# Kernel tuning notes

Measured on AMD Instinct MI355X. Metric: run time of the kernel, lower is better.

The kernel has to match this reference:

```python
import jax, jax.numpy as jnp
import numpy as np

EPS_BN = 1e-5


def conv2d(x, w, b, stride=1, pad=0):
    y = jax.lax.conv_general_dilated(
        x, w, (stride, stride), [(pad, pad), (pad, pad)],
        dimension_numbers=('NCHW', 'OIHW', 'NCHW'))
    return y + b[None, :, None, None]


def resize_ac(x, oh, ow):
    # bilinear resize, align_corners=True (matches F.interpolate(..., align_corners=True))
    N, C, H, W = x.shape
    ys = jnp.linspace(0.0, H - 1.0, oh)
    xs = jnp.linspace(0.0, W - 1.0, ow)
    y0 = jnp.floor(ys).astype(jnp.int32)
    x0 = jnp.floor(xs).astype(jnp.int32)
    y1 = jnp.minimum(y0 + 1, H - 1)
    x1 = jnp.minimum(x0 + 1, W - 1)
    wy = (ys - y0)[None, None, :, None]
    wx = (xs - x0)[None, None, None, :]
    top = jnp.take(x, y0, axis=2)
    bot = jnp.take(x, y1, axis=2)
    rows = top * (1.0 - wy) + bot * wy
    left = jnp.take(rows, x0, axis=3)
    right = jnp.take(rows, x1, axis=3)
    return left * (1.0 - wx) + right * wx


def grid_sample_3d(vol, grid):
    # vol: (N,C,D,H,W); grid: (N,Do,Ho,Wo,3) with channels (x->W, y->H, z->D)
    # trilinear, padding_mode='zeros', align_corners=False (torch defaults)
    N, C, D, H, W = vol.shape
    out_shape = grid.shape[1:4]
    gx = grid[..., 0].reshape(N, -1)
    gy = grid[..., 1].reshape(N, -1)
    gz = grid[..., 2].reshape(N, -1)
    ix = ((gx + 1.0) * W - 1.0) * 0.5
    iy = ((gy + 1.0) * H - 1.0) * 0.5
    iz = ((gz + 1.0) * D - 1.0) * 0.5
    x0 = jnp.floor(ix); y0 = jnp.floor(iy); z0 = jnp.floor(iz)
    fx = ix - x0; fy = iy - y0; fz = iz - z0
    volf = vol.reshape(N, C, D * H * W)

    def corner(xi, yi, zi, wgt):
        valid = ((xi >= 0) & (xi < W) & (yi >= 0) & (yi < H) & (zi >= 0) & (zi < D))
        xc = jnp.clip(xi, 0, W - 1).astype(jnp.int32)
        yc = jnp.clip(yi, 0, H - 1).astype(jnp.int32)
        zc = jnp.clip(zi, 0, D - 1).astype(jnp.int32)
        lin = (zc * H + yc) * W + xc  # (N,P)
        g = jnp.take_along_axis(volf, lin[:, None, :], axis=2)  # (N,C,P)
        return g * (wgt * valid.astype(vol.dtype))[:, None, :]

    out = 0.0
    for zi, wz in ((z0, 1.0 - fz), (z0 + 1.0, fz)):
        for yi, wy in ((y0, 1.0 - fy), (y0 + 1.0, fy)):
            for xi, wx in ((x0, 1.0 - fx), (x0 + 1.0, fx)):
                out = out + corner(xi, yi, zi, wz * wy * wx)
    return out.reshape(N, C, *out_shape)


def setup_inputs() -> dict:
    key = jax.random.key(0)
    ks = jax.random.split(key, 9)
    N, H, W = 1, 2048, 2048
    f = lambda k, shp, s: jax.random.normal(k, shp, jnp.float32) * s
    return dict(
        low=jax.random.uniform(ks[0], (N, 3, H, W), jnp.float32),
        med=jax.random.uniform(ks[1], (N, 3, H, W), jnp.float32),
        high=jax.random.uniform(ks[2], (N, 3, H, W), jnp.float32),
        w1=f(ks[3], (16, 9, 3, 3), 0.1), b1=jnp.zeros((16,), jnp.float32),
        w2=f(ks[4], (32, 16, 3, 3), 0.1), b2=jnp.zeros((32,), jnp.float32),
        w3=f(ks[5], (64, 32, 3, 3), 0.1), b3=jnp.zeros((64,), jnp.float32),
        w4=f(ks[6], (192, 64, 1, 1), 0.1), b4=jnp.zeros((192,), jnp.float32),
        gw1=f(ks[7], (16, 3, 1, 1), 0.3), gb1=jnp.zeros((16,), jnp.float32),
        g_gamma=jnp.ones((16,), jnp.float32), g_beta=jnp.zeros((16,), jnp.float32),
        g_mean=jnp.zeros((16,), jnp.float32), g_var=jnp.ones((16,), jnp.float32),
        gw2=f(ks[8], (1, 16, 1, 1), 0.3), gb2=jnp.zeros((1,), jnp.float32),
    )


def _forward(low, med, high, w1, b1, w2, b2, w3, b3, w4, b4,
             gw1, gb1, g_gamma, g_beta, g_mean, g_var, gw2, gb2):
    img = 0.33 * low + 0.33 * med + 0.33 * high  # (N,3,H,W)

    # ---- Coeffs: downsample 9-ch input to 128x128, run coeff net -> (N,12,16,16,16)
    x = resize_ac(jnp.concatenate([low, med, high], axis=1), 128, 128)
    x = jax.nn.relu(conv2d(x, w1, b1, stride=2, pad=1))   # 64x64
    x = jax.nn.relu(conv2d(x, w2, b2, stride=2, pad=1))   # 32x32
    x = jax.nn.relu(conv2d(x, w3, b3, stride=2, pad=1))   # 16x16
    coeff = conv2d(x, w4, b4, stride=1, pad=0)            # (N,192,16,16)
    grid_vol = coeff.reshape(-1, 12, 16, 16, 16)          # (N,12,D,H,W)

    # ---- GuideNN at full res: 1x1 conv -> BN(eval) -> ReLU -> 1x1 conv -> sigmoid
    g = conv2d(img, gw1, gb1)
    g = g_gamma[None, :, None, None] * (g - g_mean[None, :, None, None]) \
        * jax.lax.rsqrt(g_var[None, :, None, None] + EPS_BN) + g_beta[None, :, None, None]
    g = jax.nn.relu(g)
    guide = jax.nn.sigmoid(conv2d(g, gw2, gb2))           # (N,1,H,W)
    guide = resize_ac(guide, 64, 64)[:, 0]                # (N,64,64)

    # ---- Slice: trilinear lookup into bilateral grid, guided by (guide, hg, wg)
    N = guide.shape[0]
    lin = (jnp.arange(64, dtype=jnp.float32) / 63.0) * 2.0 - 1.0
    hg = jnp.broadcast_to(lin[:, None], (64, 64))
    wg = jnp.broadcast_to(lin[None, :], (64, 64))
    grid = jnp.stack([guide,
                      jnp.broadcast_to(hg, guide.shape),
                      jnp.broadcast_to(wg, guide.shape)], axis=-1)[:, None]  # (N,1,64,64,3)
    sc = grid_sample_3d(grid_vol, grid)[:, :, 0]          # (N,12,64,64)

    # ---- Apply: upsample coeffs to full res, per-pixel 3x4 affine (HDRNet apply)
    Hi, Wi = img.shape[2], img.shape[3]
    cf = resize_ac(sc, Hi, Wi).reshape(N, 3, 4, Hi, Wi)
    out = jnp.einsum('ncjhw,njhw->nchw', cf[:, :, :3], img) + cf[:, :, 3]
    return out


def reference(low, med, high, w1, b1, w2, b2, w3, b3, w4, b4,
              gw1, gb1, g_gamma, g_beta, g_mean, g_var, gw2, gb2):
    return _forward(low, med, high, w1, b1, w2, b2, w3, b3, w4, b4,
                    gw1, gb1, g_gamma, g_beta, g_mean, g_var, gw2, gb2)
```

## Files before the change

### kernel.cpp

```cpp
#include <hip/hip_runtime.h>
#include <math.h>

#define HH 2048
#define WW 2048
#define HWFULL (HH*WW)

typedef float v4f __attribute__((ext_vector_type(4)));
union F4 { float4 v; v4f c; float f[4]; };

__global__ __launch_bounds__(256) void k_conv1(const float* __restrict__ low,
                                               const float* __restrict__ med,
                                               const float* __restrict__ high,
                                               const float* __restrict__ w,
                                               const float* __restrict__ b,
                                               float* __restrict__ out) {
    __shared__ float sd[9 * 3 * 34];
    const int oy = blockIdx.x >> 2;
    const int q  = blockIdx.x & 3;
    const int tid = threadIdx.x;
    for (int idx = tid; idx < 9 * 3 * 33; idx += 256) {
        int ch = idx / 99;
        int rem = idx - 99 * ch;
        int r = rem / 33;
        int j = rem - 33 * r;
        int ix128 = 32 * q - 1 + j;
        int iy128 = 2 * oy - 1 + r;
        float val = 0.0f;
        if (ix128 >= 0 && ix128 < 128 && iy128 >= 0 && iy128 < 128) {
            const float* base = (ch < 3) ? low : (ch < 6 ? med : high);
            const float* p = base + (ch % 3) * HWFULL;
            float ysf = iy128 * (2047.0f / 127.0f);
            int y0 = (int)ysf; if (y0 > 2047) y0 = 2047;
            int y1 = y0 + 1;   if (y1 > 2047) y1 = 2047;
            float wy = ysf - (float)y0;
            float xsf = ix128 * (2047.0f / 127.0f);
            int x0 = (int)xsf; if (x0 > 2047) x0 = 2047;
            int x1 = x0 + 1;   if (x1 > 2047) x1 = 2047;
            float wx = xsf - (float)x0;
            float t = p[y0 * WW + x0] * (1.0f - wx) + p[y0 * WW + x1] * wx;
            float bo = p[y1 * WW + x0] * (1.0f - wx) + p[y1 * WW + x1] * wx;
            val = t * (1.0f - wy) + bo * wy;
        }
        sd[(ch * 3 + r) * 34 + j] = val;
    }
    __syncthreads();
    int co = tid >> 4, xl = tid & 15;
    float acc = b[co];
    for (int ci = 0; ci < 9; ++ci) {
        #pragma unroll
        for (int ky = 0; ky < 3; ++ky) {
            const float* wr = w + ((co * 9 + ci) * 3 + ky) * 3;
            const float* row = &sd[(ci * 3 + ky) * 34 + 2 * xl];
            acc += wr[0] * row[0] + wr[1] * row[1] + wr[2] * row[2];
        }
    }
    out[co * 4096 + oy * 64 + 16 * q + xl] = fmaxf(acc, 0.0f);
}

__global__ __launch_bounds__(256) void k_conv2(const float* __restrict__ in,
                                               const float* __restrict__ w,
                                               const float* __restrict__ b,
                                               const float* __restrict__ low,
                                               const float* __restrict__ med,
                                               const float* __restrict__ high,
                                               const float* __restrict__ gw1, const float* __restrict__ gb1,
                                               const float* __restrict__ gamma, const float* __restrict__ beta,
                                               const float* __restrict__ mean, const float* __restrict__ var,
                                               const float* __restrict__ gw2, const float* __restrict__ gb2,
                                               float* __restrict__ out,
                                               float* __restrict__ guideb) {
    __shared__ float sd[16 * 3 * 18];
    const int oy = blockIdx.x >> 2;
    const int q  = blockIdx.x & 3;
    const int tid = threadIdx.x;
    for (int idx = tid; idx < 16 * 3 * 17; idx += 256) {
        int ch = idx / 51;
        int rem = idx - 51 * ch;
        int r = rem / 17;
        int j = rem - 17 * r;
        int x = 16 * q - 1 + j;
        int iy = 2 * oy - 1 + r;
        sd[(ch * 3 + r) * 18 + j] =
            (x >= 0 && x < 64 && iy >= 0 && iy < 64) ? in[ch * 4096 + iy * 64 + x] : 0.0f;
    }
    __syncthreads();
    int co = tid >> 3, xl = tid & 7;
    float acc = b[co];
    for (int ci = 0; ci < 16; ++ci) {
        #pragma unroll
        for (int ky = 0; ky < 3; ++ky) {
            const float* wr = w + ((co * 16 + ci) * 3 + ky) * 3;
            const float* row = &sd[(ci * 3 + ky) * 18 + 2 * xl];
            acc += wr[0] * row[0] + wr[1] * row[1] + wr[2] * row[2];
        }
    }
    out[co * 1024 + oy * 32 + 8 * q + xl] = fmaxf(acc, 0.0f);

    if (tid < 32) {
        int g = blockIdx.x * 32 + tid;
        int h = g >> 6, wv = g & 63;
        float ysf = h * (2047.0f / 63.0f);
        int y0 = (int)ysf; if (y0 > 2047) y0 = 2047;
        int y1 = y0 + 1;   if (y1 > 2047) y1 = 2047;
        float wy = ysf - (float)y0;
        float xsf = wv * (2047.0f / 63.0f);
        int x0 = (int)xsf; if (x0 > 2047) x0 = 2047;
        int x1 = x0 + 1;   if (x1 > 2047) x1 = 2047;
        float wx = xsf - (float)x0;
        int yy[2] = { y0, y1 };
        int xx[2] = { x0, x1 };
        float gp[2][2];
        #pragma unroll
        for (int a = 0; a < 2; ++a) {
            #pragma unroll
            for (int bb = 0; bb < 2; ++bb) {
                int pix = yy[a] * WW + xx[bb];
                float i0 = 0.33f * (low[pix]            + med[pix]            + high[pix]);
                float i1 = 0.33f * (low[HWFULL + pix]   + med[HWFULL + pix]   + high[HWFULL + pix]);
                float i2 = 0.33f * (low[2*HWFULL + pix] + med[2*HWFULL + pix] + high[2*HWFULL + pix]);
                float acc2 = gb2[0];
                for (int k = 0; k < 16; ++k) {
                    float t = gb1[k] + gw1[k*3] * i0 + gw1[k*3+1] * i1 + gw1[k*3+2] * i2;
                    t = gamma[k] * (t - mean[k]) * (1.0f / sqrtf(var[k] + 1e-5f)) + beta[k];
                    t = fmaxf(t, 0.0f);
                    acc2 += gw2[k] * t;
                }
                gp[a][bb] = 1.0f / (1.0f + expf(-acc2));
            }
        }
        guideb[g] = (1.0f - wy) * ((1.0f - wx) * gp[0][0] + wx * gp[0][1])
                  +         wy  * ((1.0f - wx) * gp[1][0] + wx * gp[1][1]);
    }
}

__global__ __launch_bounds__(256) void k_conv34(const float* __restrict__ in,
                                                const float* __restrict__ w3,
                                                const float* __restrict__ b3,
                                                const float* __restrict__ w4,
                                                const float* __restrict__ b4,
                                                float* __restrict__ gridvol) {
    __shared__ float sd[32 * 3 * 10];
    __shared__ float sc3[64 * 4];
    const int oy = blockIdx.x >> 2;
    const int q  = blockIdx.x & 3;
    const int tid = threadIdx.x;
    for (int idx = tid; idx < 32 * 3 * 9; idx += 256) {
        int ch = idx / 27;
        int rem = idx - 27 * ch;
        int r = rem / 9;
        int j = rem - 9 * r;
        int x = 8 * q - 1 + j;
        int iy = 2 * oy - 1 + r;
        sd[(ch * 3 + r) * 10 + j] =
            (x >= 0 && x < 32 && iy >= 0 && iy < 32) ? in[ch * 1024 + iy * 32 + x] : 0.0f;
    }
    __syncthreads();
    {
        int co = tid >> 2, xl = tid & 3;
        float acc = b3[co];
        for (int ci = 0; ci < 32; ++ci) {
            #pragma unroll
            for (int ky = 0; ky < 3; ++ky) {
                const float* wr = w3 + ((co * 32 + ci) * 3 + ky) * 3;
                const float* row = &sd[(ci * 3 + ky) * 10 + 2 * xl];
                acc += wr[0] * row[0] + wr[1] * row[1] + wr[2] * row[2];
            }
        }
        sc3[co * 4 + xl] = fmaxf(acc, 0.0f);
    }
    __syncthreads();
    {
        int px = tid & 3;
        int ob = tid >> 2;
        #pragma unroll
        for (int k = 0; k < 3; ++k) {
            int o = ob + 64 * k;
            float sum = b4[o];
            const float* wp = w4 + o * 64;
            for (int i = 0; i < 64; ++i)
                sum += wp[i] * sc3[i * 4 + px];
            gridvol[o * 256 + oy * 16 + 4 * q + px] = sum;
        }
    }
}

__global__ __launch_bounds__(256) void k_slice_ab(
        const float* __restrict__ gridvol, const float* __restrict__ guideb,
        float* __restrict__ ab_full) {
    __shared__ float s[3 * 64 * 12];
    const int b = blockIdx.x;
    const int tid = threadIdx.x;
    float byf = (8 * b) * (63.0f / 2047.0f);
    int v0 = (int)byf; if (v0 > 63) v0 = 63;

    if (tid < 192) {
        int rr = tid >> 6, x = tid & 63;
        int srow = v0 + rr; if (srow > 63) srow = 63;
        float guide = guideb[srow * 64 + x];
        float hg = srow * (2.0f / 63.0f) - 1.0f;
        float wg = x * (2.0f / 63.0f) - 1.0f;
        float ix = ((guide + 1.0f) * 16.0f - 1.0f) * 0.5f;
        float iy = ((hg    + 1.0f) * 16.0f - 1.0f) * 0.5f;
        float iz = ((wg    + 1.0f) * 16.0f - 1.0f) * 0.5f;
        float xf = floorf(ix), yf = floorf(iy), zf = floorf(iz);
        float fx = ix - xf, fyy = iy - yf, fz = iz - zf;
        int xi = (int)xf, yi = (int)yf, zi = (int)zf;
        float scv[12];
        #pragma unroll
        for (int c = 0; c < 12; ++c) scv[c] = 0.0f;
        #pragma unroll
        for (int dz = 0; dz < 2; ++dz) {
            int z = zi + dz; float wz = dz ? fz : 1.0f - fz;
            if (z < 0 || z > 15) continue;
            #pragma unroll
            for (int dy = 0; dy < 2; ++dy) {
                int yv = yi + dy; float wyv = dy ? fyy : 1.0f - fyy;
                if (yv < 0 || yv > 15) continue;
                #pragma unroll
                for (int dx = 0; dx < 2; ++dx) {
                    int xv = xi + dx; float wxv = dx ? fx : 1.0f - fx;
                    if (xv < 0 || xv > 15) continue;
                    float wgt = wz * wyv * wxv;
                    int base = yv * 16 + xv;
                    #pragma unroll
                    for (int c = 0; c < 12; ++c)
                        scv[c] += wgt * gridvol[(c * 16 + z) * 256 + base];
                }
            }
        }
        #pragma unroll
        for (int c = 0; c < 12; ++c) s[(rr * 64 + x) * 12 + c] = scv[c];
    }
    __syncthreads();

    #pragma unroll
    for (int k = 0; k < 24; ++k) {
        int e = k * 256 + tid;
        int r8 = e / 768;
        int rem = e - 768 * r8;
        int x = rem / 12;
        int c = rem - 12 * x;
        int y = 8 * b + r8;
        float iyf = y * (63.0f / 2047.0f);
        int y0 = (int)iyf; if (y0 > 63) y0 = 63;
        int y1 = y0 + 1;   if (y1 > 63) y1 = 63;
        float fy = iyf - (float)y0;
        int i0 = y0 - v0, i1 = y1 - v0;
        float t = s[(i0 * 64 + x) * 12 + c];
        float bo = s[(i1 * 64 + x) * 12 + c];
        ab_full[y * 768 + rem] = t + (bo - t) * fy;
    }
}

__global__ __launch_bounds__(256) void k_apply(
        const float* __restrict__ low, const float* __restrict__ med,
        const float* __restrict__ high, const float* __restrict__ ab_full,
        float* __restrict__ out) {
    const int g = blockIdx.x * 256 + threadIdx.x;
    const int y = g >> 9;
    const int v = g & 511;
    const int HW4 = HWFULL / 4;

    const float4* Lp = (const float4*)low;
    const float4* Mp = (const float4*)med;
    const float4* Hp = (const float4*)high;

    F4 l0, l1, l2, m0, m1, m2, h0, h1, h2;
    l0.v = Lp[g]; l1.v = Lp[g + HW4]; l2.v = Lp[g + 2 * HW4];
    m0.v = Mp[g]; m1.v = Mp[g + HW4]; m2.v = Mp[g + 2 * HW4];
    h0.v = Hp[g]; h1.v = Hp[g + HW4]; h2.v = Hp[g + 2 * HW4];

    const float4* abr = (const float4*)(ab_full + y * 768);
    int x_first = v << 2;
    float ixf0 = x_first * (63.0f / 2047.0f);
    int f = (int)ixf0; if (f > 63) f = 63;
    float ixf3 = (x_first + 3) * (63.0f / 2047.0f);
    int s3 = (int)ixf3; if (s3 > 63) s3 = 63;
    int fp1 = f + 1;  if (fp1 > 63) fp1 = 63;
    int sp1 = s3 + 1; if (sp1 > 63) sp1 = 63;
    F4 A0[3], B0[3], C0[3];
    #pragma unroll
    for (int qq = 0; qq < 3; ++qq) {
        A0[qq].v = abr[f   * 3 + qq];
        B0[qq].v = abr[fp1 * 3 + qq];
        C0[qq].v = abr[sp1 * 3 + qq];
    }

    F4 o0, o1, o2;
    #pragma unroll
    for (int p = 0; p < 4; ++p) {
        int x = x_first + p;
        float ixf = x * (63.0f / 2047.0f);
        int x0 = (int)ixf; if (x0 > 63) x0 = 63;
        float fx = ixf - (float)x0;
        bool first = (x0 == f);
        float im0 = 0.33f * (l0.f[p] + m0.f[p] + h0.f[p]);
        float im1 = 0.33f * (l1.f[p] + m1.f[p] + h1.f[p]);
        float im2 = 0.33f * (l2.f[p] + m2.f[p] + h2.f[p]);
        float cf[12];
        #pragma unroll
        for (int qq = 0; qq < 3; ++qq) {
            #pragma unroll
            for (int r = 0; r < 4; ++r) {
                float a = first ? A0[qq].f[r] : B0[qq].f[r];
                float bb = first ? B0[qq].f[r] : C0[qq].f[r];
                cf[qq * 4 + r] = a + (bb - a) * fx;
            }
        }
        o0.f[p] = cf[0] * im0 + cf[1]  * im1 + cf[2]  * im2 + cf[3];
        o1.f[p] = cf[4] * im0 + cf[5]  * im1 + cf[6]  * im2 + cf[7];
        o2.f[p] = cf[8] * im0 + cf[9]  * im1 + cf[10] * im2 + cf[11];
    }
    float4* Op = (float4*)out;
    Op[g]           = o0.v;
    Op[g + HW4]     = o1.v;
    Op[g + 2 * HW4] = o2.v;
}

extern "C" void kernel_launch(void* const* d_in, const int* in_sizes, int n_in,
                              void* d_out, int out_size, void* d_ws, size_t ws_size,
                              hipStream_t stream) {
    const float* low   = (const float*)d_in[0];
    const float* med   = (const float*)d_in[1];
    const float* high  = (const float*)d_in[2];
    const float* w1    = (const float*)d_in[3];
    const float* b1    = (const float*)d_in[4];
    const float* w2    = (const float*)d_in[5];
    const float* b2    = (const float*)d_in[6];
    const float* w3    = (const float*)d_in[7];
    const float* b3    = (const float*)d_in[8];
    const float* w4    = (const float*)d_in[9];
    const float* b4    = (const float*)d_in[10];
    const float* gw1   = (const float*)d_in[11];
    const float* gb1   = (const float*)d_in[12];
    const float* gamma = (const float*)d_in[13];
    const float* beta  = (const float*)d_in[14];
    const float* mean  = (const float*)d_in[15];
    const float* var   = (const float*)d_in[16];
    const float* gw2   = (const float*)d_in[17];
    const float* gb2   = (const float*)d_in[18];
    float* out = (float*)d_out;

    float* ws      = (float*)d_ws;
    float* ab_full = ws;
    float* c1      = ab_full + 1572864;
    float* c2v     = c1 + 65536;
    float* gridvol = c2v + 32768;
    float* guideb  = gridvol + 49152;

    hipLaunchKernelGGL(k_conv1,    dim3(256), dim3(256), 0, stream,
                       low, med, high, w1, b1, c1);
    hipLaunchKernelGGL(k_conv2,    dim3(128), dim3(256), 0, stream,
                       c1, w2, b2, low, med, high,
                       gw1, gb1, gamma, beta, mean, var, gw2, gb2, c2v, guideb);
    hipLaunchKernelGGL(k_conv34,   dim3(64),  dim3(256), 0, stream, c2v, w3, b3, w4, b4, gridvol);
    hipLaunchKernelGGL(k_slice_ab, dim3(256), dim3(256), 0, stream, gridvol, guideb, ab_full);
    hipLaunchKernelGGL(k_apply,    dim3(4096), dim3(256), 0, stream, low, med, high, ab_full, out);
}
```

Baseline: 81.20 us.

## Restructure apply kernel: one row per block, stage coeffs and image in LDS

The apply kernel now processes one full image row per block, staging that row's 192 coefficient float4s and the averaged 3-channel intensity in shared memory before computing outputs. Input loads and output stores use nontemporal builtins, and the grid is halved to 2048 blocks with two float4 outputs per thread. The aim is to cut redundant global reads of the coefficient row and reduce cache pollution on the streaming image traffic. In exchange it adds a block-wide barrier and extra LDS traffic.

```diff
diff --git a/kernel.cpp b/kernel.cpp
--- a/kernel.cpp
+++ b/kernel.cpp
@@ -256,65 +256,89 @@
         const float* __restrict__ low, const float* __restrict__ med,
         const float* __restrict__ high, const float* __restrict__ ab_full,
         float* __restrict__ out) {
-    const int g = blockIdx.x * 256 + threadIdx.x;
-    const int y = g >> 9;
-    const int v = g & 511;
+    __shared__ F4 img[3][512];
+    __shared__ F4 abs4[192];
+    const int y = blockIdx.x;
+    const int tid = threadIdx.x;
     const int HW4 = HWFULL / 4;
-
-    const float4* Lp = (const float4*)low;
-    const float4* Mp = (const float4*)med;
-    const float4* Hp = (const float4*)high;
-
-    F4 l0, l1, l2, m0, m1, m2, h0, h1, h2;
-    l0.v = Lp[g]; l1.v = Lp[g + HW4]; l2.v = Lp[g + 2 * HW4];
-    m0.v = Mp[g]; m1.v = Mp[g + HW4]; m2.v = Mp[g + 2 * HW4];
-    h0.v = Hp[g]; h1.v = Hp[g + HW4]; h2.v = Hp[g + 2 * HW4];
-
-    const float4* abr = (const float4*)(ab_full + y * 768);
-    int x_first = v << 2;
-    float ixf0 = x_first * (63.0f / 2047.0f);
-    int f = (int)ixf0; if (f > 63) f = 63;
-    float ixf3 = (x_first + 3) * (63.0f / 2047.0f);
-    int s3 = (int)ixf3; if (s3 > 63) s3 = 63;
-    int fp1 = f + 1;  if (fp1 > 63) fp1 = 63;
-    int sp1 = s3 + 1; if (sp1 > 63) sp1 = 63;
-    F4 A0[3], B0[3], C0[3];
+    const int base = y << 9;
+
+    const v4f* Lp = (const v4f*)low;
+    const v4f* Mp = (const v4f*)med;
+    const v4f* Hp = (const v4f*)high;
+
+    if (tid < 192)
+        abs4[tid].v = ((const float4*)(ab_full + y * 768))[tid];
+
     #pragma unroll
-    for (int qq = 0; qq < 3; ++qq) {
-        A0[qq].v = abr[f   * 3 + qq];
-        B0[qq].v = abr[fp1 * 3 + qq];
-        C0[qq].v = abr[sp1 * 3 + qq];
-    }
-
-    F4 o0, o1, o2;
+    for (int ch = 0; ch < 3; ++ch) {
+        int vi = base + ch * HW4 + tid;
+        F4 a, b, g, d, e, h;
+        a.c = __builtin_nontemporal_load(Lp + vi);
+        b.c = __builtin_nontemporal_load(Mp + vi);
+        g.c = __builtin_nontemporal_load(Hp + vi);
+        d.c = __builtin_nontemporal_load(Lp + vi + 256);
+        e.c = __builtin_nontemporal_load(Mp + vi + 256);
+        h.c = __builtin_nontemporal_load(Hp + vi + 256);
+        F4 r0, r1;
+        #pragma unroll
+        for (int p = 0; p < 4; ++p) {
+            r0.f[p] = 0.33f * (a.f[p] + b.f[p] + g.f[p]);
+            r1.f[p] = 0.33f * (d.f[p] + e.f[p] + h.f[p]);
+        }
+        img[ch][tid] = r0;
+        img[ch][tid + 256] = r1;
+        __builtin_amdgcn_sched_barrier(0);
+    }
+    __syncthreads();
+
+    v4f* Op = (v4f*)out;
     #pragma unroll
-    for (int p = 0; p < 4; ++p) {
-        int x = x_first + p;
-        float ixf = x * (63.0f / 2047.0f);
-        int x0 = (int)ixf; if (x0 > 63) x0 = 63;
-        float fx = ixf - (float)x0;
-        bool first = (x0 == f);
-        float im0 = 0.33f * (l0.f[p] + m0.f[p] + h0.f[p]);
-        float im1 = 0.33f * (l1.f[p] + m1.f[p] + h1.f[p]);
-        float im2 = 0.33f * (l2.f[p] + m2.f[p] + h2.f[p]);
-        float cf[12];
+    for (int q = 0; q < 2; ++q) {
+        int v = tid + q * 256;
+        int vi = base + v;
+        int x_first = v << 2;
+        float ixf0 = x_first * (63.0f / 2047.0f);
+        int f = (int)ixf0; if (f > 63) f = 63;
+        float ixf3 = (x_first + 3) * (63.0f / 2047.0f);
+        int s3 = (int)ixf3; if (s3 > 63) s3 = 63;
+        int fp1 = f + 1;  if (fp1 > 63) fp1 = 63;
+        int sp1 = s3 + 1; if (sp1 > 63) sp1 = 63;
+        F4 A0[3], B0[3], C0[3];
         #pragma unroll
         for (int qq = 0; qq < 3; ++qq) {
+            A0[qq] = abs4[f   * 3 + qq];
+            B0[qq] = abs4[fp1 * 3 + qq];
+            C0[qq] = abs4[sp1 * 3 + qq];
+        }
+        F4 i0 = img[0][v], i1 = img[1][v], i2 = img[2][v];
+
+        F4 o0, o1, o2;
+        #pragma unroll
+        for (int p = 0; p < 4; ++p) {
+            int x = x_first + p;
+            float ixf = x * (63.0f / 2047.0f);
+            int x0 = (int)ixf; if (x0 > 63) x0 = 63;
+            float fx = ixf - (float)x0;
+            bool first = (x0 == f);
+            float cf[12];
             #pragma unroll
-            for (int r = 0; r < 4; ++r) {
-                float a = first ? A0[qq].f[r] : B0[qq].f[r];
-                float bb = first ? B0[qq].f[r] : C0[qq].f[r];
-                cf[qq * 4 + r] = a + (bb - a) * fx;
+            for (int qq = 0; qq < 3; ++qq) {
+                #pragma unroll
+                for (int r = 0; r < 4; ++r) {
+                    float a = first ? A0[qq].f[r] : B0[qq].f[r];
+                    float bb = first ? B0[qq].f[r] : C0[qq].f[r];
+                    cf[qq * 4 + r] = a + (bb - a) * fx;
+                }
             }
-        }
-        o0.f[p] = cf[0] * im0 + cf[1]  * im1 + cf[2]  * im2 + cf[3];
-        o1.f[p] = cf[4] * im0 + cf[5]  * im1 + cf[6]  * im2 + cf[7];
-        o2.f[p] = cf[8] * im0 + cf[9]  * im1 + cf[10] * im2 + cf[11];
-    }
-    float4* Op = (float4*)out;
-    Op[g]           = o0.v;
-    Op[g + HW4]     = o1.v;
-    Op[g + 2 * HW4] = o2.v;
+            o0.f[p] = cf[0] * i0.f[p] + cf[1]  * i1.f[p] + cf[2]  * i2.f[p] + cf[3];
+            o1.f[p] = cf[4] * i0.f[p] + cf[5]  * i1.f[p] + cf[6]  * i2.f[p] + cf[7];
+            o2.f[p] = cf[8] * i0.f[p] + cf[9]  * i1.f[p] + cf[10] * i2.f[p] + cf[11];
+        }
+        __builtin_nontemporal_store(o0.c, Op + vi);
+        __builtin_nontemporal_store(o1.c, Op + vi + HW4);
+        __builtin_nontemporal_store(o2.c, Op + vi + 2 * HW4);
+    }
 }
 
 extern "C" void kernel_launch(void* const* d_in, const int* in_sizes, int n_in,
@@ -355,5 +379,5 @@
                        gw1, gb1, gamma, beta, mean, var, gw2, gb2, c2v, guideb);
     hipLaunchKernelGGL(k_conv34,   dim3(64),  dim3(256), 0, stream, c2v, w3, b3, w4, b4, gridvol);
     hipLaunchKernelGGL(k_slice_ab, dim3(256), dim3(256), 0, stream, gridvol, guideb, ab_full);
-    hipLaunchKernelGGL(k_apply,    dim3(4096), dim3(256), 0, stream, low, med, high, ab_full, out);
-}
+    hipLaunchKernelGGL(k_apply,    dim3(2048), dim3(256), 0, stream, low, med, high, ab_full, out);
+}
```

Result: slower. 87.33 us (+7.5%).

## Fuse conv1-conv4 into one halo-recomputing kernel and move guide into slice

Applied to the files above, without the earlier changes.

Merges the three conv kernels into a single 64-block kernel where each block recomputes its receptive-field halo (downsample, conv1, conv2) in shared memory before conv3 and the 1x1 conv4. The guide-network evaluation moves into k_slice_ab, so each slice block computes the guide values it needs instead of reading them from a buffer. This removes two launches and the global round trips for c1, c2 and guideb. In exchange it adds redundant halo compute, runs only 64 blocks for the conv chain, and repeats guide evaluations across neighbouring slice blocks.

```diff
diff --git a/kernel.cpp b/kernel.cpp
--- a/kernel.cpp
+++ b/kernel.cpp
@@ -8,105 +8,158 @@
 typedef float v4f __attribute__((ext_vector_type(4)));
 union F4 { float4 v; v4f c; float f[4]; };
 
-__global__ __launch_bounds__(256) void k_conv1(const float* __restrict__ low,
-                                               const float* __restrict__ med,
-                                               const float* __restrict__ high,
-                                               const float* __restrict__ w,
-                                               const float* __restrict__ b,
-                                               float* __restrict__ out) {
-    __shared__ float sd[9 * 3 * 34];
+__device__ __forceinline__ float bilin(const float* __restrict__ p, int yy, int xx,
+                                       float scale) {
+    float ysf = yy * scale;
+    int y0 = (int)ysf; if (y0 > 2047) y0 = 2047;
+    int y1 = y0 + 1;   if (y1 > 2047) y1 = 2047;
+    float wy = ysf - (float)y0;
+    float xsf = xx * scale;
+    int x0 = (int)xsf; if (x0 > 2047) x0 = 2047;
+    int x1 = x0 + 1;   if (x1 > 2047) x1 = 2047;
+    float wx = xsf - (float)x0;
+    float t = p[y0 * WW + x0] * (1.0f - wx) + p[y0 * WW + x1] * wx;
+    float b = p[y1 * WW + x0] * (1.0f - wx) + p[y1 * WW + x1] * wx;
+    return t * (1.0f - wy) + b * wy;
+}
+
+__global__ __launch_bounds__(256) void k_coeff(
+        const float* __restrict__ low, const float* __restrict__ med,
+        const float* __restrict__ high,
+        const float* __restrict__ w1, const float* __restrict__ b1,
+        const float* __restrict__ w2, const float* __restrict__ b2,
+        const float* __restrict__ w3, const float* __restrict__ b3,
+        const float* __restrict__ w4, const float* __restrict__ b4,
+        float* __restrict__ gridvol) {
+    __shared__ float ds9s[9][15][40];
+    __shared__ float c1s[16][7][20];
+    __shared__ float c2s[32][3][10];
+    __shared__ float c3s[64][4];
     const int oy = blockIdx.x >> 2;
     const int q  = blockIdx.x & 3;
     const int tid = threadIdx.x;
-    for (int idx = tid; idx < 9 * 3 * 33; idx += 256) {
-        int ch = idx / 99;
-        int rem = idx - 99 * ch;
-        int r = rem / 33;
-        int j = rem - 33 * r;
-        int ix128 = 32 * q - 1 + j;
-        int iy128 = 2 * oy - 1 + r;
+
+    for (int idx = tid; idx < 9 * 15 * 39; idx += 256) {
+        int ch = idx / 585;
+        int rem = idx - 585 * ch;
+        int r = rem / 39;
+        int j = rem - 39 * r;
+        int yy = 8 * oy - 7 + r;
+        int xx = 32 * q - 7 + j;
         float val = 0.0f;
-        if (ix128 >= 0 && ix128 < 128 && iy128 >= 0 && iy128 < 128) {
+        if (yy >= 0 && yy < 128 && xx >= 0 && xx < 128) {
             const float* base = (ch < 3) ? low : (ch < 6 ? med : high);
-            const float* p = base + (ch % 3) * HWFULL;
-            float ysf = iy128 * (2047.0f / 127.0f);
-            int y0 = (int)ysf; if (y0 > 2047) y0 = 2047;
-            int y1 = y0 + 1;   if (y1 > 2047) y1 = 2047;
-            float wy = ysf - (float)y0;
-            float xsf = ix128 * (2047.0f / 127.0f);
-            int x0 = (int)xsf; if (x0 > 2047) x0 = 2047;
-            int x1 = x0 + 1;   if (x1 > 2047) x1 = 2047;
-            float wx = xsf - (float)x0;
-            float t = p[y0 * WW + x0] * (1.0f - wx) + p[y0 * WW + x1] * wx;
-            float bo = p[y1 * WW + x0] * (1.0f - wx) + p[y1 * WW + x1] * wx;
-            val = t * (1.0f - wy) + bo * wy;
-        }
-        sd[(ch * 3 + r) * 34 + j] = val;
-    }
-    __syncthreads();
-    int co = tid >> 4, xl = tid & 15;
-    float acc = b[co];
-    for (int ci = 0; ci < 9; ++ci) {
-        #pragma unroll
-        for (int ky = 0; ky < 3; ++ky) {
-            const float* wr = w + ((co * 9 + ci) * 3 + ky) * 3;
-            const float* row = &sd[(ci * 3 + ky) * 34 + 2 * xl];
-            acc += wr[0] * row[0] + wr[1] * row[1] + wr[2] * row[2];
-        }
-    }
-    out[co * 4096 + oy * 64 + 16 * q + xl] = fmaxf(acc, 0.0f);
-}
-
-__global__ __launch_bounds__(256) void k_conv2(const float* __restrict__ in,
-                                               const float* __restrict__ w,
-                                               const float* __restrict__ b,
-                                               const float* __restrict__ low,
-                                               const float* __restrict__ med,
-                                               const float* __restrict__ high,
-                                               const float* __restrict__ gw1, const float* __restrict__ gb1,
-                                               const float* __restrict__ gamma, const float* __restrict__ beta,
-                                               const float* __restrict__ mean, const float* __restrict__ var,
-                                               const float* __restrict__ gw2, const float* __restrict__ gb2,
-                                               float* __restrict__ out,
-                                               float* __restrict__ guideb) {
-    __shared__ float sd[16 * 3 * 18];
-    const int oy = blockIdx.x >> 2;
-    const int q  = blockIdx.x & 3;
+            val = bilin(base + (ch % 3) * HWFULL, yy, xx, 2047.0f / 127.0f);
+        }
+        ds9s[ch][r][j] = val;
+    }
+    __syncthreads();
+
+    for (int v = tid; v < 16 * 7 * 19; v += 256) {
+        int co = v / 133;
+        int rem = v - 133 * co;
+        int r = rem / 19;
+        int x = rem - 19 * r;
+        int Y = 4 * oy - 3 + r;
+        int X = 16 * q - 3 + x;
+        float val = 0.0f;
+        if (Y >= 0 && Y < 64 && X >= 0 && X < 64) {
+            float acc = b1[co];
+            for (int ci = 0; ci < 9; ++ci) {
+                #pragma unroll
+                for (int ky = 0; ky < 3; ++ky) {
+                    const float* wr = w1 + ((co * 9 + ci) * 3 + ky) * 3;
+                    const float* row = &ds9s[ci][2 * r + ky][2 * x];
+                    acc += wr[0] * row[0] + wr[1] * row[1] + wr[2] * row[2];
+                }
+            }
+            val = fmaxf(acc, 0.0f);
+        }
+        c1s[co][r][x] = val;
+    }
+    __syncthreads();
+
+    for (int v = tid; v < 32 * 3 * 9; v += 256) {
+        int co = v / 27;
+        int rem = v - 27 * co;
+        int r = rem / 9;
+        int x = rem - 9 * r;
+        int Y = 2 * oy - 1 + r;
+        int X = 8 * q - 1 + x;
+        float val = 0.0f;
+        if (Y >= 0 && Y < 32 && X >= 0 && X < 32) {
+            float acc = b2[co];
+            for (int ci = 0; ci < 16; ++ci) {
+                #pragma unroll
+                for (int ky = 0; ky < 3; ++ky) {
+                    const float* wr = w2 + ((co * 16 + ci) * 3 + ky) * 3;
+                    const float* row = &c1s[ci][2 * r + ky][2 * x];
+                    acc += wr[0] * row[0] + wr[1] * row[1] + wr[2] * row[2];
+                }
+            }
+            val = fmaxf(acc, 0.0f);
+        }
+        c2s[co][r][x] = val;
+    }
+    __syncthreads();
+
+    {
+        int co = tid >> 2, xl = tid & 3;
+        float acc = b3[co];
+        for (int ci = 0; ci < 32; ++ci) {
+            #pragma unroll
+            for (int ky = 0; ky < 3; ++ky) {
+                const float* wr = w3 + ((co * 32 + ci) * 3 + ky) * 3;
+                const float* row = &c2s[ci][ky][2 * xl];
+                acc += wr[0] * row[0] + wr[1] * row[1] + wr[2] * row[2];
+            }
+        }
+        c3s[co][xl] = fmaxf(acc, 0.0f);
+    }
+    __syncthreads();
+
+    {
+        int px = tid & 3;
+        int ob = tid >> 2;
+        #pragma unroll
+        for (int k = 0; k < 3; ++k) {
+            int o = ob + 64 * k;
+            float sum = b4[o];
+            const float* wp = w4 + o * 64;
+            for (int i = 0; i < 64; ++i)
+                sum += wp[i] * c3s[i][px];
+            gridvol[o * 256 + oy * 16 + 4 * q + px] = sum;
+        }
+    }
+}
+
+__global__ __launch_bounds__(256) void k_slice_ab(
+        const float* __restrict__ gridvol,
+        const float* __restrict__ low, const float* __restrict__ med,
+        const float* __restrict__ high,
+        const float* __restrict__ gw1, const float* __restrict__ gb1,
+        const float* __restrict__ gamma, const float* __restrict__ beta,
+        const float* __restrict__ mean, const float* __restrict__ var,
+        const float* __restrict__ gw2, const float* __restrict__ gb2,
+        float* __restrict__ ab_full) {
+    __shared__ float s[3 * 64 * 12];
+    const int b = blockIdx.x;
     const int tid = threadIdx.x;
-    for (int idx = tid; idx < 16 * 3 * 17; idx += 256) {
-        int ch = idx / 51;
-        int rem = idx - 51 * ch;
-        int r = rem / 17;
-        int j = rem - 17 * r;
-        int x = 16 * q - 1 + j;
-        int iy = 2 * oy - 1 + r;
-        sd[(ch * 3 + r) * 18 + j] =
-            (x >= 0 && x < 64 && iy >= 0 && iy < 64) ? in[ch * 4096 + iy * 64 + x] : 0.0f;
-    }
-    __syncthreads();
-    int co = tid >> 3, xl = tid & 7;
-    float acc = b[co];
-    for (int ci = 0; ci < 16; ++ci) {
-        #pragma unroll
-        for (int ky = 0; ky < 3; ++ky) {
-            const float* wr = w + ((co * 16 + ci) * 3 + ky) * 3;
-            const float* row = &sd[(ci * 3 + ky) * 18 + 2 * xl];
-            acc += wr[0] * row[0] + wr[1] * row[1] + wr[2] * row[2];
-        }
-    }
-    out[co * 1024 + oy * 32 + 8 * q + xl] = fmaxf(acc, 0.0f);
-
-    if (tid < 32) {
-        int g = blockIdx.x * 32 + tid;
-        int h = g >> 6, wv = g & 63;
-        float ysf = h * (2047.0f / 63.0f);
+    float byf = (8 * b) * (63.0f / 2047.0f);
+    int v0 = (int)byf; if (v0 > 63) v0 = 63;
+
+    if (tid < 192) {
+        int rr = tid >> 6, x = tid & 63;
+        int srow = v0 + rr; if (srow > 63) srow = 63;
+
+        float ysf = srow * (2047.0f / 63.0f);
         int y0 = (int)ysf; if (y0 > 2047) y0 = 2047;
         int y1 = y0 + 1;   if (y1 > 2047) y1 = 2047;
-        float wy = ysf - (float)y0;
-        float xsf = wv * (2047.0f / 63.0f);
+        float wyg = ysf - (float)y0;
+        float xsf = x * (2047.0f / 63.0f);
         int x0 = (int)xsf; if (x0 > 2047) x0 = 2047;
         int x1 = x0 + 1;   if (x1 > 2047) x1 = 2047;
-        float wx = xsf - (float)x0;
+        float wxg = xsf - (float)x0;
         int yy[2] = { y0, y1 };
         int xx[2] = { x0, x1 };
         float gp[2][2];
@@ -128,75 +181,9 @@
                 gp[a][bb] = 1.0f / (1.0f + expf(-acc2));
             }
         }
-        guideb[g] = (1.0f - wy) * ((1.0f - wx) * gp[0][0] + wx * gp[0][1])
-                  +         wy  * ((1.0f - wx) * gp[1][0] + wx * gp[1][1]);
-    }
-}
-
-__global__ __launch_bounds__(256) void k_conv34(const float* __restrict__ in,
-                                                const float* __restrict__ w3,
-                                                const float* __restrict__ b3,
-                                                const float* __restrict__ w4,
-                                                const float* __restrict__ b4,
-                                                float* __restrict__ gridvol) {
-    __shared__ float sd[32 * 3 * 10];
-    __shared__ float sc3[64 * 4];
-    const int oy = blockIdx.x >> 2;
-    const int q  = blockIdx.x & 3;
-    const int tid = threadIdx.x;
-    for (int idx = tid; idx < 32 * 3 * 9; idx += 256) {
-        int ch = idx / 27;
-        int rem = idx - 27 * ch;
-        int r = rem / 9;
-        int j = rem - 9 * r;
-        int x = 8 * q - 1 + j;
-        int iy = 2 * oy - 1 + r;
-        sd[(ch * 3 + r) * 10 + j] =
-            (x >= 0 && x < 32 && iy >= 0 && iy < 32) ? in[ch * 1024 + iy * 32 + x] : 0.0f;
-    }
-    __syncthreads();
-    {
-        int co = tid >> 2, xl = tid & 3;
-        float acc = b3[co];
-        for (int ci = 0; ci < 32; ++ci) {
-            #pragma unroll
-            for (int ky = 0; ky < 3; ++ky) {
-                const float* wr = w3 + ((co * 32 + ci) * 3 + ky) * 3;
-                const float* row = &sd[(ci * 3 + ky) * 10 + 2 * xl];
-                acc += wr[0] * row[0] + wr[1] * row[1] + wr[2] * row[2];
-            }
-        }
-        sc3[co * 4 + xl] = fmaxf(acc, 0.0f);
-    }
-    __syncthreads();
-    {
-        int px = tid & 3;
-        int ob = tid >> 2;
-        #pragma unroll
-        for (int k = 0; k < 3; ++k) {
-            int o = ob + 64 * k;
-            float sum = b4[o];
-            const float* wp = w4 + o * 64;
-            for (int i = 0; i < 64; ++i)
-                sum += wp[i] * sc3[i * 4 + px];
-            gridvol[o * 256 + oy * 16 + 4 * q + px] = sum;
-        }
-    }
-}
-
-__global__ __launch_bounds__(256) void k_slice_ab(
-        const float* __restrict__ gridvol, const float* __restrict__ guideb,
-        float* __restrict__ ab_full) {
-    __shared__ float s[3 * 64 * 12];
-    const int b = blockIdx.x;
-    const int tid = threadIdx.x;
-    float byf = (8 * b) * (63.0f / 2047.0f);
-    int v0 = (int)byf; if (v0 > 63) v0 = 63;
-
-    if (tid < 192) {
-        int rr = tid >> 6, x = tid & 63;
-        int srow = v0 + rr; if (srow > 63) srow = 63;
-        float guide = guideb[srow * 64 + x];
+        float guide = (1.0f - wyg) * ((1.0f - wxg) * gp[0][0] + wxg * gp[0][1])
+                    +         wyg  * ((1.0f - wxg) * gp[1][0] + wxg * gp[1][1]);
+
         float hg = srow * (2.0f / 63.0f) - 1.0f;
         float wg = x * (2.0f / 63.0f) - 1.0f;
         float ix = ((guide + 1.0f) * 16.0f - 1.0f) * 0.5f;
@@ -343,17 +330,13 @@
 
     float* ws      = (float*)d_ws;
     float* ab_full = ws;
-    float* c1      = ab_full + 1572864;
-    float* c2v     = c1 + 65536;
-    float* gridvol = c2v + 32768;
-    float* guideb  = gridvol + 49152;
-
-    hipLaunchKernelGGL(k_conv1,    dim3(256), dim3(256), 0, stream,
-                       low, med, high, w1, b1, c1);
-    hipLaunchKernelGGL(k_conv2,    dim3(128), dim3(256), 0, stream,
-                       c1, w2, b2, low, med, high,
-                       gw1, gb1, gamma, beta, mean, var, gw2, gb2, c2v, guideb);
-    hipLaunchKernelGGL(k_conv34,   dim3(64),  dim3(256), 0, stream, c2v, w3, b3, w4, b4, gridvol);
-    hipLaunchKernelGGL(k_slice_ab, dim3(256), dim3(256), 0, stream, gridvol, guideb, ab_full);
-    hipLaunchKernelGGL(k_apply,    dim3(4096), dim3(256), 0, stream, low, med, high, ab_full, out);
-}
+    float* gridvol = ab_full + 1572864;
+
+    hipLaunchKernelGGL(k_coeff,    dim3(64),  dim3(256), 0, stream,
+                       low, med, high, w1, b1, w2, b2, w3, b3, w4, b4, gridvol);
+    hipLaunchKernelGGL(k_slice_ab, dim3(256), dim3(256), 0, stream,
+                       gridvol, low, med, high,
+                       gw1, gb1, gamma, beta, mean, var, gw2, gb2, ab_full);
+    hipLaunchKernelGGL(k_apply,    dim3(4096), dim3(256), 0, stream,
+                       low, med, high, ab_full, out);
+}
```

After: 104.1 us. +28.2%, slower.
